# Optimization experiments

Hardware: AMD Instinct MI355X
Metric: run time of the kernel (lower is better)

The kernel has to match this reference:

```python
import jax, jax.numpy as jnp
import numpy as np

B, T, C = 4, 2048, 2048
H, HKV, D = 16, 8, 128
SECTIONS = (24, 20, 20)  # sums to 64 = D/2 -> full-dim rotation branch
EPS = 1e-6


def setup_inputs() -> dict:
    key = jax.random.key(0)
    ks = jax.random.split(key, 8)
    x = jax.random.normal(ks[0], (B, T, C), dtype=jnp.float32)
    # realistic RoPE tables: [3, B, T, 64] (3 mRoPE axes: t/h/w)
    half = sum(SECTIONS)  # 64
    inv_freq = 1.0 / (10000.0 ** (jnp.arange(half, dtype=jnp.float32) / half))
    pos = jnp.arange(T, dtype=jnp.float32)
    freqs = pos[:, None] * inv_freq[None, :]                      # [T, 64]
    freqs3 = jnp.broadcast_to(freqs, (3, B, T, half))
    # small per-axis offsets so the three mRoPE axes differ
    axis_off = jnp.arange(3, dtype=jnp.float32)[:, None, None, None] * 0.5
    cos = jnp.cos(freqs3 + axis_off)
    sin = jnp.sin(freqs3 + axis_off)
    mask = jnp.ones((B, T), dtype=jnp.int32)
    s = 1.0 / np.sqrt(C)
    Wq = jax.random.normal(ks[1], (C, H * D), dtype=jnp.float32) * s
    Wk = jax.random.normal(ks[2], (C, HKV * D), dtype=jnp.float32) * s
    Wv = jax.random.normal(ks[3], (C, HKV * D), dtype=jnp.float32) * s
    Wo = jax.random.normal(ks[4], (H * D, C), dtype=jnp.float32) * (1.0 / np.sqrt(H * D))
    return dict(x=x, cos=cos, sin=sin, mask=mask,
                Wq=Wq, bq=jnp.zeros((H * D,), jnp.float32),
                Wk=Wk, bk=jnp.zeros((HKV * D,), jnp.float32),
                Wv=Wv, bv=jnp.zeros((HKV * D,), jnp.float32),
                gq=jnp.ones((D,), jnp.float32), gk=jnp.ones((D,), jnp.float32),
                Wo=Wo)


def _rms_norm(x, gamma, eps):
    var = jnp.mean(jnp.square(x.astype(jnp.float32)), axis=-1, keepdims=True)
    return (gamma * x * jax.lax.rsqrt(var + eps)).astype(x.dtype)


def _rotate_half(x):
    x1, x2 = jnp.split(x, 2, axis=-1)
    return jnp.concatenate((-x2, x1), axis=-1)


def _reorder(table):
    # interleave mRoPE sections: take section i from axis i, then duplicate
    chunks, off = [], 0
    for i, sec in enumerate(SECTIONS):
        chunks.append(table[i, ..., off:off + sec])
        off += sec
    r = jnp.concatenate(chunks, axis=-1)        # [B, T, 64]
    return jnp.concatenate([r, r], axis=-1)     # [B, T, 128]


def reference(x, cos, sin, mask, Wq, bq, Wk, bk, Wv, bv, gq, gk, Wo):
    b, t = x.shape[0], x.shape[1]
    q = (x @ Wq + bq).reshape(b, t, H, D)
    k = (x @ Wk + bk).reshape(b, t, HKV, D)
    v = (x @ Wv + bv).reshape(b, t, HKV, D)
    q = _rms_norm(q, gq, EPS)
    k = _rms_norm(k, gk, EPS)
    q = jnp.transpose(q, (0, 2, 1, 3))   # [B, H, T, D]
    k = jnp.transpose(k, (0, 2, 1, 3))   # [B, HKV, T, D]
    v = jnp.transpose(v, (0, 2, 1, 3))
    cos_e = _reorder(cos)[:, None].astype(q.dtype)  # [B, 1, T, D]
    sin_e = _reorder(sin)[:, None].astype(q.dtype)
    q = q * cos_e + _rotate_half(q) * sin_e
    k = k * cos_e + _rotate_half(k) * sin_e
    key_mask = mask.astype(jnp.float32)                         # [B, T]
    lengths = key_mask.sum(axis=-1).astype(jnp.int32)           # [B]
    k = k * key_mask[:, None, :, None].astype(k.dtype)
    v = v * key_mask[:, None, :, None].astype(v.dtype)
    history_mask = (jnp.arange(t)[None, :] < lengths[:, None]).astype(jnp.float32)
    repeats = H // HKV
    qg = q.reshape(b, HKV, repeats, t, D)
    scores = jnp.einsum('bhgqd,bhkd->bhgqk', qg.astype(jnp.float32),
                        k.astype(jnp.float32)) * D ** -0.5
    scores = scores.reshape(b, H, t, t)
    scores = scores + (1.0 - history_mask)[:, None, None, :] * -1e9
    causal = jnp.tril(jnp.ones((t, t), dtype=jnp.float32))
    scores = scores + (1.0 - causal)[None, None] * -1e9
    weights = jax.nn.softmax(scores, axis=-1)
    wg = weights.reshape(b, HKV, repeats, t, t)
    out = jnp.einsum('bhgqk,bhkd->bhgqd', wg, v.astype(jnp.float32))
    out = out.reshape(b, H, t, D).astype(x.dtype)
    out = jnp.transpose(out, (0, 2, 1, 3)).reshape(b, t, H * D)
    return out @ Wo
```

## Files before the change

kernel.cpp:

```cpp
#include <hip/hip_runtime.h>
#include <stdint.h>

#define B_    4
#define T_    2048
#define C_    2048
#define H_    16
#define HKV_  8
#define D_    128
#define HD_   2048
#define KVD_  1024
#define NQKV_ 4096
#define BT_   8192

typedef __bf16 bf16x8 __attribute__((ext_vector_type(8)));
typedef float  f32x4  __attribute__((ext_vector_type(4)));
typedef unsigned short u16;
typedef unsigned int   u32;

__device__ __forceinline__ u16 f2b(float f){
  union { float f; u32 u; } v; v.f = f;
  u32 r = v.u + 0x7FFFu + ((v.u >> 16) & 1u);
  return (u16)(r >> 16);
}
__device__ __forceinline__ float b2f(u16 h){
  union { u32 u; float f; } v; v.u = ((u32)h) << 16;
  return v.f;
}

#define GLOAD16(src, dst) __builtin_amdgcn_global_load_lds( \
    (const __attribute__((address_space(1))) u32*)(src), \
    (__attribute__((address_space(3))) u32*)(dst), 16, 0, 0)

#define MFMA16(a,b,c) __builtin_amdgcn_mfma_f32_16x16x32_bf16((a), (b), (c), 0, 0, 0)

__global__ __launch_bounds__(256) void k_convx(const float* __restrict__ x, u16* __restrict__ xb){
  size_t i = ((size_t)blockIdx.x * 256 + threadIdx.x) * 4;
  float4 v = *(const float4*)(x + i);
  u32 w0 = (u32)f2b(v.x) | ((u32)f2b(v.y) << 16);
  u32 w1 = (u32)f2b(v.z) | ((u32)f2b(v.w) << 16);
  uint2 pk; pk.x = w0; pk.y = w1;
  *(uint2*)(xb + i) = pk;
}

__global__ __launch_bounds__(256) void k_wtrans(const float* __restrict__ src, u16* __restrict__ dst,
                                                int K, int N){
  __shared__ __attribute__((aligned(16))) u16 tile[64][68];
  int n0 = blockIdx.x * 64, k0 = blockIdx.y * 64;
  int r = threadIdx.x >> 4, c4 = (threadIdx.x & 15) * 4;
  #pragma unroll
  for (int rr = 0; rr < 4; ++rr){
    int kl = r + rr * 16;
    float4 v = *(const float4*)(src + (size_t)(k0 + kl) * N + n0 + c4);
    tile[kl][c4+0] = f2b(v.x); tile[kl][c4+1] = f2b(v.y);
    tile[kl][c4+2] = f2b(v.z); tile[kl][c4+3] = f2b(v.w);
  }
  __syncthreads();
  #pragma unroll
  for (int rr = 0; rr < 4; ++rr){
    int nl = r + rr * 16;
    u32 w0 = (u32)tile[c4+0][nl] | ((u32)tile[c4+1][nl] << 16);
    u32 w1 = (u32)tile[c4+2][nl] | ((u32)tile[c4+3][nl] << 16);
    uint2 pk; pk.x = w0; pk.y = w1;
    *(uint2*)(dst + (size_t)(n0 + nl) * K + k0 + c4) = pk;
  }
}

__global__ void k_prep(const float* __restrict__ bq, const float* __restrict__ bk,
                       const float* __restrict__ bv, float* __restrict__ bias){
  int i = blockIdx.x * 256 + threadIdx.x;
  if (i < NQKV_)
    bias[i] = (i < HD_) ? bq[i] : (i < HD_ + KVD_ ? bk[i - HD_] : bv[i - HD_ - KVD_]);
}

__global__ void k_lens(const int* __restrict__ mask, int* __restrict__ lens){
  int b = blockIdx.x;
  int s = 0;
  for (int t = threadIdx.x; t < T_; t += 256) s += mask[b * T_ + t];
  #pragma unroll
  for (int d = 1; d < 64; d <<= 1) s += __shfl_xor(s, d);
  __shared__ int acc[4];
  if ((threadIdx.x & 63) == 0) acc[threadIdx.x >> 6] = s;
  __syncthreads();
  if (threadIdx.x == 0) lens[b] = acc[0] + acc[1] + acc[2] + acc[3];
}

template<bool OUTF32>
__global__ __launch_bounds__(512, 2) void k_gemm(const u16* __restrict__ A, const u16* __restrict__ BT,
                                                 const float* __restrict__ bias, void* __restrict__ Cout,
                                                 int M, int N, int K, int nbx){
  __shared__ __attribute__((aligned(16))) u16 As[2][256 * 64];
  __shared__ __attribute__((aligned(16))) u16 Bs[2][256 * 64];
  int nwg = gridDim.x;
  int fid = blockIdx.x;
  int gs = (fid & 7) * (nwg >> 3) + (fid >> 3);
  int bx = gs % nbx, by = gs / nbx;
  int m0 = by * 256, n0 = bx * 256;
  int tid = threadIdx.x;
  int lane = tid & 63, w = tid >> 6;
  int wm = w >> 2, wn = w & 3;
  int g = lane >> 4, lo = lane & 15;
  int lsx = (lo & 7) << 3;
  int wgb = tid & 448;
  f32x4 acc[8][4] = {};

  auto STAGE_HALF = [&](const u16* __restrict__ src, int k0, u16* lds){
    #pragma unroll
    for (int i = 0; i < 2; ++i){
      int gI = i * 512 + tid;
      int row = gI >> 3, grp = gI & 7;
      GLOAD16(src + (size_t)row * K + k0 + ((grp ^ (row & 7)) << 3),
              &lds[(i * 512 + wgb) * 8]);
    }
  };
  auto STAGE_TILE = [&](int k0, int bufi){
    STAGE_HALF(A  + (size_t)m0 * K,          k0, &As[bufi][0]);
    STAGE_HALF(A  + (size_t)(m0 + 128) * K,  k0, &As[bufi][8192]);
    STAGE_HALF(BT + (size_t)n0 * K,          k0, &Bs[bufi][0]);
    STAGE_HALF(BT + (size_t)(n0 + 128) * K,  k0, &Bs[bufi][8192]);
  };

  int nk = K >> 6;
  STAGE_TILE(0, 0);
  for (int t = 0; t < nk; ++t){
    int cur = t & 1, nxt = cur ^ 1;
    bool pf = (t + 1 < nk);
    if (pf){
      STAGE_TILE((t + 1) * 64, nxt);
      asm volatile("s_waitcnt vmcnt(8)" ::: "memory");
    } else {
      asm volatile("s_waitcnt vmcnt(0)" ::: "memory");
    }
    __builtin_amdgcn_s_barrier();
    __builtin_amdgcn_sched_barrier(0);
    bf16x8 bfr[4][2];
    #pragma unroll
    for (int nr = 0; nr < 4; ++nr){
      bfr[nr][0] = *(const bf16x8*)&Bs[cur][(wn*64 + nr*16 + lo) * 64 + ((0*32 + g*8) ^ lsx)];
      bfr[nr][1] = *(const bf16x8*)&Bs[cur][(wn*64 + nr*16 + lo) * 64 + ((1*32 + g*8) ^ lsx)];
    }
    __builtin_amdgcn_s_setprio(1);
    #pragma unroll
    for (int p = 0; p < 4; ++p){
      int r0 = 2 * p, r1 = 2 * p + 1;
      bf16x8 a00 = *(const bf16x8*)&As[cur][(wm*128 + r0*16 + lo) * 64 + ((0*32 + g*8) ^ lsx)];
      bf16x8 a01 = *(const bf16x8*)&As[cur][(wm*128 + r0*16 + lo) * 64 + ((1*32 + g*8) ^ lsx)];
      bf16x8 a10 = *(const bf16x8*)&As[cur][(wm*128 + r1*16 + lo) * 64 + ((0*32 + g*8) ^ lsx)];
      bf16x8 a11 = *(const bf16x8*)&As[cur][(wm*128 + r1*16 + lo) * 64 + ((1*32 + g*8) ^ lsx)];
      #pragma unroll
      for (int nr = 0; nr < 4; ++nr){
        acc[r0][nr] = MFMA16(a00, bfr[nr][0], acc[r0][nr]);
        acc[r0][nr] = MFMA16(a01, bfr[nr][1], acc[r0][nr]);
        acc[r1][nr] = MFMA16(a10, bfr[nr][0], acc[r1][nr]);
        acc[r1][nr] = MFMA16(a11, bfr[nr][1], acc[r1][nr]);
      }
    }
    __builtin_amdgcn_s_setprio(0);
    __builtin_amdgcn_s_barrier();
  }
  #pragma unroll
  for (int mr = 0; mr < 8; ++mr){
    #pragma unroll
    for (int nr = 0; nr < 4; ++nr){
      #pragma unroll
      for (int r = 0; r < 4; ++r){
        int row = m0 + wm*128 + mr*16 + g*4 + r;
        int col = n0 + wn*64 + nr*16 + lo;
        float v = acc[mr][nr][r] + (bias ? bias[col] : 0.0f);
        if (OUTF32) ((float*)Cout)[(size_t)row * N + col] = v;
        else        ((u16*)Cout)[(size_t)row * N + col] = f2b(v);
      }
    }
  }
}

__global__ __launch_bounds__(256) void k_rmsrope(const u16* __restrict__ qkv,
    const float* __restrict__ cosp, const float* __restrict__ sinp,
    const int* __restrict__ mask, const float* __restrict__ gq, const float* __restrict__ gk,
    u16* __restrict__ qrot, u16* __restrict__ krot){
  const float QS = 0.08838834764831845f * 1.4426950408889634f;
  int tok = blockIdx.x;
  int b = tok >> 11, t = tok & (T_ - 1);
  int lane = threadIdx.x & 63, w = threadIdx.x >> 6;
  int dl = (lane & 31) * 2;
  int a0 = dl < 24 ? 0 : (dl < 44 ? 1 : 2);
  int a1 = (dl + 1) < 24 ? 0 : ((dl + 1) < 44 ? 1 : 2);
  size_t cb = ((size_t)b * T_ + t) * 64;
  const size_t AX = (size_t)B_ * T_ * 64;
  float ce0 = cosp[(size_t)a0 * AX + cb + dl],     se0 = sinp[(size_t)a0 * AX + cb + dl];
  float ce1 = cosp[(size_t)a1 * AX + cb + dl + 1], se1 = sinp[(size_t)a1 * AX + cb + dl + 1];
  float sgn = (lane < 32) ? -1.f : 1.f;
  float mk = (float)mask[b * T_ + t];
  const u16* base = qkv + (size_t)tok * NQKV_;
  for (int head = w; head < H_ + HKV_; head += 4){
    bool isq = head < H_;
    int off = isq ? head * D_ : HD_ + (head - H_) * D_;
    u32 pr = *(const u32*)(base + off + lane * 2);
    float x0 = b2f((u16)(pr & 0xFFFF)), x1 = b2f((u16)(pr >> 16));
    float ss = x0*x0 + x1*x1;
    #pragma unroll
    for (int d = 1; d < 64; d <<= 1) ss += __shfl_xor(ss, d);
    float rinv = rsqrtf(ss * (1.0f / 128.0f) + 1e-6f);
    const float* gg = isq ? gq : gk;
    float2 gv = *(const float2*)(gg + lane * 2);
    float n0 = gv.x * x0 * rinv, n1 = gv.y * x1 * rinv;
    float p0 = __shfl_xor(n0, 32), p1 = __shfl_xor(n1, 32);
    float o0 = n0 * ce0 + sgn * p0 * se0;
    float o1 = n1 * ce1 + sgn * p1 * se1;
    u16* dst;
    if (isq){
      o0 *= QS; o1 *= QS;
      dst = qrot + ((size_t)(b * H_ + head) * T_ + t) * D_;
    } else {
      o0 *= mk; o1 *= mk;
      dst = krot + ((size_t)(b * HKV_ + (head - H_)) * T_ + t) * D_;
    }
    u32 ow = (u32)f2b(o0) | ((u32)f2b(o1) << 16);
    *(u32*)(dst + lane * 2) = ow;
  }
}

__global__ __launch_bounds__(256) void k_vtrans(const u16* __restrict__ qkv, const int* __restrict__ mask,
                                                u16* __restrict__ vt){
  int t0 = blockIdx.x * 64, d0 = blockIdx.y * 64;
  int bh = blockIdx.z;
  int b = bh >> 3, hk = bh & 7;
  __shared__ __attribute__((aligned(16))) u16 tile[64][68];
  int r = threadIdx.x >> 4, c4 = (threadIdx.x & 15) * 4;
  #pragma unroll
  for (int rr = 0; rr < 4; ++rr){
    int tl = r + rr * 16;
    int t = t0 + tl;
    u16 mz = (u16)(mask[b * T_ + t] ? 0xFFFFu : 0u);
    ushort4 v = *(const ushort4*)(qkv + (size_t)(b * T_ + t) * NQKV_ + HD_ + KVD_ + hk * D_ + d0 + c4);
    tile[tl][c4+0] = (u16)(v.x & mz); tile[tl][c4+1] = (u16)(v.y & mz);
    tile[tl][c4+2] = (u16)(v.z & mz); tile[tl][c4+3] = (u16)(v.w & mz);
  }
  __syncthreads();
  #pragma unroll
  for (int rr = 0; rr < 4; ++rr){
    int dn = r + rr * 16;
    u32 w0 = (u32)tile[c4+0][dn] | ((u32)tile[c4+1][dn] << 16);
    u32 w1 = (u32)tile[c4+2][dn] | ((u32)tile[c4+3][dn] << 16);
    uint2 pk; pk.x = w0; pk.y = w1;
    *(uint2*)(vt + ((size_t)bh * D_ + d0 + dn) * T_ + t0 + c4) = pk;
  }
}

__global__ __launch_bounds__(512) void k_attn(const u16* __restrict__ qrot, const u16* __restrict__ krot,
                                              const u16* __restrict__ vt, const int* __restrict__ lens,
                                              u16* __restrict__ ao){
  int fid = blockIdx.x;
  int gs = (fid & 7) * 128 + (fid >> 3);
  int qi = (gs & 15) ^ 15;
  int q0 = qi * 128;
  int h = (gs >> 4) & 15, b = gs >> 8;
  int hk = h >> 1;
  int tid = threadIdx.x;
  int lane = tid & 63, w = tid >> 6;
  int g = lane >> 4, lo = lane & 15;
  int len = lens[b];
  __shared__ __attribute__((aligned(16))) u16 Ks[2][64 * 128];
  __shared__ __attribute__((aligned(16))) u16 Vs[2][128 * 64];
  const u16* qbase = qrot + ((size_t)(b * H_ + h) * T_ + q0 + w * 16 + lo) * D_ + g * 8;
  bf16x8 qf[4];
  #pragma unroll
  for (int kk = 0; kk < 4; ++kk) qf[kk] = *(const bf16x8*)(qbase + kk * 32);
  float m_run = -1e30f, l_run = 0.f;
  f32x4 o[8] = {};
  int qrow = q0 + w * 16 + lo;
  const u16* kbase = krot + (size_t)(b * HKV_ + hk) * T_ * D_;
  const u16* vbase = vt   + (size_t)(b * HKV_ + hk) * D_ * T_;
  int wbase = tid & 448;
  int lsx = (lo & 7) << 3;
  int srcA = ((lane & 16) * 2 + lo) * 4;
  int srcB = srcA + 64;
  bool hiL = lane >= 32;

  auto STAGE = [&](int j0, int bufi){
    #pragma unroll
    for (int i = 0; i < 2; ++i){
      int gI = i * 512 + tid;
      int row = gI >> 4, grp = gI & 15;
      GLOAD16(kbase + (size_t)(j0 + row) * D_ + ((grp ^ (row & 7)) << 3),
              &Ks[bufi][(i * 512 + wbase) * 8]);
    }
    #pragma unroll
    for (int i = 0; i < 2; ++i){
      int gI = i * 512 + tid;
      int row = gI >> 3, grp = gI & 7;
      GLOAD16(vbase + (size_t)row * T_ + j0 + ((grp ^ (row & 7)) << 3),
              &Vs[bufi][(i * 512 + wbase) * 8]);
    }
  };

  STAGE(0, 0);
  int cur = 0;
  int jend = q0 + 64;
  for (int j0 = 0; j0 <= jend && j0 < len; j0 += 64){
    int jn = j0 + 64;
    bool hasnext = (jn <= jend && jn < len);
    if (hasnext){
      STAGE(jn, cur ^ 1);
      asm volatile("s_waitcnt vmcnt(4)" ::: "memory");
    } else {
      asm volatile("s_waitcnt vmcnt(0)" ::: "memory");
    }
    __builtin_amdgcn_s_barrier();
    __builtin_amdgcn_sched_barrier(0);
    bool wlive = (j0 <= q0 + w * 16 + 15);
    if (wlive){
      f32x4 st[4] = {};
      __builtin_amdgcn_s_setprio(1);
      #pragma unroll
      for (int kk = 0; kk < 4; ++kk){
        #pragma unroll
        for (int nf = 0; nf < 4; ++nf){
          bf16x8 kf = *(const bf16x8*)&Ks[cur][(nf * 16 + lo) * 128 + ((kk * 32 + g * 8) ^ lsx)];
          st[nf] = MFMA16(kf, qf[kk], st[nf]);
        }
      }
      __builtin_amdgcn_s_setprio(0);
      bool needmask = (j0 + 63 > q0 + w * 16) || (j0 + 64 > len);
      if (needmask){
        #pragma unroll
        for (int nf = 0; nf < 4; ++nf)
          #pragma unroll
          for (int r = 0; r < 4; ++r){
            int k = j0 + nf * 16 + g * 4 + r;
            if (k > qrow || k >= len) st[nf][r] = -1e30f;
          }
      }
      float mf[4];
      #pragma unroll
      for (int nf = 0; nf < 4; ++nf)
        mf[nf] = fmaxf(fmaxf(st[nf][0], st[nf][1]), fmaxf(st[nf][2], st[nf][3]));
      float mx = fmaxf(fmaxf(mf[0], mf[1]), fmaxf(mf[2], mf[3]));
      mx = fmaxf(mx, __shfl_xor(mx, 16));
      mx = fmaxf(mx, __shfl_xor(mx, 32));
      bool skip = __all(mx <= m_run + 8.0f);
      float mn = skip ? m_run : fmaxf(m_run, mx);
      float sf[4];
      #pragma unroll
      for (int nf = 0; nf < 4; ++nf){
        #pragma unroll
        for (int r = 0; r < 4; ++r){
          float e = exp2f(st[nf][r] - mn);
          st[nf][r] = e;
        }
        sf[nf] = (st[nf][0] + st[nf][1]) + (st[nf][2] + st[nf][3]);
      }
      float sum = (sf[0] + sf[1]) + (sf[2] + sf[3]);
      sum += __shfl_xor(sum, 16);
      sum += __shfl_xor(sum, 32);
      if (skip){
        l_run += sum;
      } else {
        float alpha = exp2f(m_run - mn);
        l_run = l_run * alpha + sum;
        m_run = mn;
        #pragma unroll
        for (int r = 0; r < 4; ++r){
          float ar = __shfl(alpha, (lane & 48) | ((g * 4 + r) & 15));
          #pragma unroll
          for (int df = 0; df < 8; ++df) o[df][r] *= ar;
        }
      }
      u32 pk[4][2];
      #pragma unroll
      for (int nf = 0; nf < 4; ++nf){
        union { u32 u; __bf16 hh[2]; } c0, c1;
        c0.hh[0] = (__bf16)st[nf][0]; c0.hh[1] = (__bf16)st[nf][1];
        c1.hh[0] = (__bf16)st[nf][2]; c1.hh[1] = (__bf16)st[nf][3];
        pk[nf][0] = c0.u; pk[nf][1] = c1.u;
      }
      #pragma unroll
      for (int kk2 = 0; kk2 < 2; ++kk2){
        u32 a0 = (u32)__builtin_amdgcn_ds_bpermute(srcA, (int)pk[2*kk2][0]);
        u32 b0 = (u32)__builtin_amdgcn_ds_bpermute(srcA, (int)pk[2*kk2+1][0]);
        u32 a1 = (u32)__builtin_amdgcn_ds_bpermute(srcA, (int)pk[2*kk2][1]);
        u32 b1 = (u32)__builtin_amdgcn_ds_bpermute(srcA, (int)pk[2*kk2+1][1]);
        u32 a2 = (u32)__builtin_amdgcn_ds_bpermute(srcB, (int)pk[2*kk2][0]);
        u32 b2 = (u32)__builtin_amdgcn_ds_bpermute(srcB, (int)pk[2*kk2+1][0]);
        u32 a3 = (u32)__builtin_amdgcn_ds_bpermute(srcB, (int)pk[2*kk2][1]);
        u32 b3 = (u32)__builtin_amdgcn_ds_bpermute(srcB, (int)pk[2*kk2+1][1]);
        union { u32 u[4]; bf16x8 v; } pf;
        pf.u[0] = hiL ? b0 : a0;
        pf.u[1] = hiL ? b1 : a1;
        pf.u[2] = hiL ? b2 : a2;
        pf.u[3] = hiL ? b3 : a3;
        __builtin_amdgcn_s_setprio(1);
        #pragma unroll
        for (int df = 0; df < 8; ++df){
          bf16x8 vf = *(const bf16x8*)&Vs[cur][(df * 16 + lo) * 64 + ((kk2 * 32 + g * 8) ^ lsx)];
          o[df] = MFMA16(pf.v, vf, o[df]);
        }
        __builtin_amdgcn_s_setprio(0);
      }
    }
    __builtin_amdgcn_s_barrier();
    cur ^= 1;
  }
  #pragma unroll
  for (int r = 0; r < 4; ++r){
    float lr = __shfl(l_run, (lane & 48) | ((g * 4 + r) & 15));
    float rl = 1.0f / lr;
    int row = q0 + w * 16 + g * 4 + r;
    #pragma unroll
    for (int df = 0; df < 8; ++df){
      float ov = o[df][r] * rl;
      ao[((size_t)(b * T_ + row)) * HD_ + h * D_ + df * 16 + lo] = f2b(ov);
    }
  }
}

extern "C" void kernel_launch(void* const* d_in, const int* in_sizes, int n_in,
                              void* d_out, int out_size, void* d_ws, size_t ws_size,
                              hipStream_t stream) {
  (void)in_sizes; (void)n_in; (void)out_size; (void)ws_size;
  const float* x    = (const float*)d_in[0];
  const float* cosp = (const float*)d_in[1];
  const float* sinp = (const float*)d_in[2];
  const int*   mask = (const int*)d_in[3];
  const float* Wq   = (const float*)d_in[4];
  const float* bq   = (const float*)d_in[5];
  const float* Wk   = (const float*)d_in[6];
  const float* bk   = (const float*)d_in[7];
  const float* Wv   = (const float*)d_in[8];
  const float* bv   = (const float*)d_in[9];
  const float* gq   = (const float*)d_in[10];
  const float* gk   = (const float*)d_in[11];
  const float* Wo   = (const float*)d_in[12];

  char* ws = (char*)d_ws;
  const size_t MB = 1024 * 1024;
  u16*   XB    = (u16*)(ws);
  u16*   WQKVT = (u16*)(ws + 32  * MB);
  u16*   WOT   = (u16*)(ws + 48  * MB);
  u16*   QKV   = (u16*)(ws + 56  * MB);
  u16*   QROT  = (u16*)(ws + 120 * MB);
  u16*   KROT  = (u16*)(ws + 152 * MB);
  u16*   VT    = (u16*)(ws + 168 * MB);
  u16*   AO    = (u16*)(ws + 184 * MB);
  float* BIAS  = (float*)(ws + 216 * MB);
  int*   LENS  = (int*)(ws + 216 * MB + 65536);

  k_convx<<<16384, 256, 0, stream>>>(x, XB);
  k_wtrans<<<dim3(32, 32), 256, 0, stream>>>(Wq, WQKVT, C_, HD_);
  k_wtrans<<<dim3(16, 32), 256, 0, stream>>>(Wk, WQKVT + (size_t)HD_ * C_, C_, KVD_);
  k_wtrans<<<dim3(16, 32), 256, 0, stream>>>(Wv, WQKVT + (size_t)(HD_ + KVD_) * C_, C_, KVD_);
  k_wtrans<<<dim3(32, 32), 256, 0, stream>>>(Wo, WOT, HD_, C_);
  k_prep<<<16, 256, 0, stream>>>(bq, bk, bv, BIAS);
  k_lens<<<4, 256, 0, stream>>>(mask, LENS);

  k_gemm<false><<<512, 512, 0, stream>>>(XB, WQKVT, BIAS, QKV, BT_, NQKV_, C_, 16);
  k_rmsrope<<<BT_, 256, 0, stream>>>(QKV, cosp, sinp, mask, gq, gk, QROT, KROT);
  k_vtrans<<<dim3(T_ / 64, D_ / 64, B_ * HKV_), 256, 0, stream>>>(QKV, mask, VT);
  k_attn<<<1024, 512, 0, stream>>>(QROT, KROT, VT, LENS, AO);
  k_gemm<true><<<256, 512, 0, stream>>>(AO, WOT, nullptr, d_out, BT_, C_, HD_, 8);
}
```

Measured before the change: 491.5 us.

## Split GEMM K-tile into four staged phases with finer-grained prefetch waits

```diff
diff --git a/kernel.cpp b/kernel.cpp
--- a/kernel.cpp
+++ b/kernel.cpp
@@ -85,11 +85,11 @@
 }
 
 template<bool OUTF32>
-__global__ __launch_bounds__(512, 2) void k_gemm(const u16* __restrict__ A, const u16* __restrict__ BT,
-                                                 const float* __restrict__ bias, void* __restrict__ Cout,
-                                                 int M, int N, int K, int nbx){
-  __shared__ __attribute__((aligned(16))) u16 As[2][256 * 64];
-  __shared__ __attribute__((aligned(16))) u16 Bs[2][256 * 64];
+__global__ __launch_bounds__(512) void k_gemm(const u16* __restrict__ A, const u16* __restrict__ BT,
+                                              const float* __restrict__ bias, void* __restrict__ Cout,
+                                              int M, int N, int K, int nbx){
+  __shared__ __attribute__((aligned(16))) u16 As[2][2][8192];
+  __shared__ __attribute__((aligned(16))) u16 Bs[2][2][8192];
   int nwg = gridDim.x;
   int fid = blockIdx.x;
   int gs = (fid & 7) * (nwg >> 3) + (fid >> 3);
@@ -99,72 +99,77 @@
   int lane = tid & 63, w = tid >> 6;
   int wm = w >> 2, wn = w & 3;
   int g = lane >> 4, lo = lane & 15;
-  int lsx = (lo & 7) << 3;
   int wgb = tid & 448;
   f32x4 acc[8][4] = {};
 
-  auto STAGE_HALF = [&](const u16* __restrict__ src, int k0, u16* lds){
+  auto STAGE_HALF = [&](const u16* __restrict__ src, int kbase, u16* lds){
     #pragma unroll
     for (int i = 0; i < 2; ++i){
       int gI = i * 512 + tid;
-      int row = gI >> 3, grp = gI & 7;
-      GLOAD16(src + (size_t)row * K + k0 + ((grp ^ (row & 7)) << 3),
+      int row = gI >> 2, gsl = gI & 3;
+      int sw = (row >> 1) & 3;
+      GLOAD16(src + (size_t)row * K + kbase + ((gsl ^ sw) << 3),
               &lds[(i * 512 + wgb) * 8]);
     }
   };
-  auto STAGE_TILE = [&](int k0, int bufi){
-    STAGE_HALF(A  + (size_t)m0 * K,          k0, &As[bufi][0]);
-    STAGE_HALF(A  + (size_t)(m0 + 128) * K,  k0, &As[bufi][8192]);
-    STAGE_HALF(BT + (size_t)n0 * K,          k0, &Bs[bufi][0]);
-    STAGE_HALF(BT + (size_t)(n0 + 128) * K,  k0, &Bs[bufi][8192]);
+  auto ISSUE = [&](int kt, int h, int b){
+    int kbase = kt * 64 + (h >> 1) * 32;
+    if ((h & 1) == 0) STAGE_HALF(A  + (size_t)m0 * K, kbase, &As[b][h >> 1][0]);
+    else              STAGE_HALF(BT + (size_t)n0 * K, kbase, &Bs[b][h >> 1][0]);
   };
 
   int nk = K >> 6;
-  STAGE_TILE(0, 0);
+  ISSUE(0, 0, 0); ISSUE(0, 1, 0); ISSUE(0, 2, 0); ISSUE(0, 3, 0);
   for (int t = 0; t < nk; ++t){
     int cur = t & 1, nxt = cur ^ 1;
     bool pf = (t + 1 < nk);
-    if (pf){
-      STAGE_TILE((t + 1) * 64, nxt);
-      asm volatile("s_waitcnt vmcnt(8)" ::: "memory");
-    } else {
-      asm volatile("s_waitcnt vmcnt(0)" ::: "memory");
-    }
-    __builtin_amdgcn_s_barrier();
-    __builtin_amdgcn_sched_barrier(0);
-    bf16x8 bfr[4][2];
+    bf16x8 bfr[4];
+    #pragma unroll
+    for (int p = 0; p < 4; ++p){
+      if (pf) ISSUE(t + 1, p, nxt);
+      if (p == 0){
+        if (pf) asm volatile("s_waitcnt vmcnt(6)" ::: "memory");
+        else    asm volatile("s_waitcnt vmcnt(4)" ::: "memory");
+      } else if (p == 2){
+        if (pf) asm volatile("s_waitcnt vmcnt(6)" ::: "memory");
+        else    asm volatile("s_waitcnt vmcnt(0)" ::: "memory");
+      }
+      __builtin_amdgcn_s_barrier();
+      __builtin_amdgcn_sched_barrier(0);
+      int kh = p >> 1, mh = p & 1;
+      if (mh == 0){
+        #pragma unroll
+        for (int nf = 0; nf < 4; ++nf){
+          int brow = wn * 64 + nf * 16 + lo;
+          int sw = (brow >> 1) & 3;
+          bfr[nf] = *(const bf16x8*)&Bs[cur][kh][brow * 32 + ((g ^ sw) << 3)];
+        }
+      }
+      bf16x8 af[4];
+      #pragma unroll
+      for (int i = 0; i < 4; ++i){
+        int arow = wm * 128 + (mh * 4 + i) * 16 + lo;
+        int sw = (arow >> 1) & 3;
+        af[i] = *(const bf16x8*)&As[cur][kh][arow * 32 + ((g ^ sw) << 3)];
+      }
+      __builtin_amdgcn_s_setprio(1);
+      #pragma unroll
+      for (int i = 0; i < 4; ++i)
+        #pragma unroll
+        for (int nf = 0; nf < 4; ++nf)
+          acc[mh * 4 + i][nf] = MFMA16(af[i], bfr[nf], acc[mh * 4 + i][nf]);
+      __builtin_amdgcn_s_setprio(0);
+      __builtin_amdgcn_s_barrier();
+    }
+  }
+  #pragma unroll
+  for (int mr = 0; mr < 8; ++mr){
     #pragma unroll
     for (int nr = 0; nr < 4; ++nr){
-      bfr[nr][0] = *(const bf16x8*)&Bs[cur][(wn*64 + nr*16 + lo) * 64 + ((0*32 + g*8) ^ lsx)];
-      bfr[nr][1] = *(const bf16x8*)&Bs[cur][(wn*64 + nr*16 + lo) * 64 + ((1*32 + g*8) ^ lsx)];
-    }
-    __builtin_amdgcn_s_setprio(1);
-    #pragma unroll
-    for (int p = 0; p < 4; ++p){
-      int r0 = 2 * p, r1 = 2 * p + 1;
-      bf16x8 a00 = *(const bf16x8*)&As[cur][(wm*128 + r0*16 + lo) * 64 + ((0*32 + g*8) ^ lsx)];
-      bf16x8 a01 = *(const bf16x8*)&As[cur][(wm*128 + r0*16 + lo) * 64 + ((1*32 + g*8) ^ lsx)];
-      bf16x8 a10 = *(const bf16x8*)&As[cur][(wm*128 + r1*16 + lo) * 64 + ((0*32 + g*8) ^ lsx)];
-      bf16x8 a11 = *(const bf16x8*)&As[cur][(wm*128 + r1*16 + lo) * 64 + ((1*32 + g*8) ^ lsx)];
-      #pragma unroll
-      for (int nr = 0; nr < 4; ++nr){
-        acc[r0][nr] = MFMA16(a00, bfr[nr][0], acc[r0][nr]);
-        acc[r0][nr] = MFMA16(a01, bfr[nr][1], acc[r0][nr]);
-        acc[r1][nr] = MFMA16(a10, bfr[nr][0], acc[r1][nr]);
-        acc[r1][nr] = MFMA16(a11, bfr[nr][1], acc[r1][nr]);
-      }
-    }
-    __builtin_amdgcn_s_setprio(0);
-    __builtin_amdgcn_s_barrier();
-  }
-  #pragma unroll
-  for (int mr = 0; mr < 8; ++mr){
-    #pragma unroll
-    for (int nr = 0; nr < 4; ++nr){
       #pragma unroll
       for (int r = 0; r < 4; ++r){
-        int row = m0 + wm*128 + mr*16 + g*4 + r;
-        int col = n0 + wn*64 + nr*16 + lo;
+        int row = m0 + wm * 128 + mr * 16 + g * 4 + r;
+        int col = n0 + wn * 64 + nr * 16 + lo;
         float v = acc[mr][nr][r] + (bias ? bias[col] : 0.0f);
         if (OUTF32) ((float*)Cout)[(size_t)row * N + col] = v;
         else        ((u16*)Cout)[(size_t)row * N + col] = f2b(v);
```

Measured after the change: 526.1 us. 7.1% more time.
